# Performance work log

Hardware: AMD Instinct MI355X
Metric: run time of the kernel (lower is better)

The kernel has to match this reference:

```python
import jax, jax.numpy as jnp
import numpy as np
import math

FEATURE_DIMS = 6
D_HIDDEN = 32
N_TOKENS = 2097152
NUM_SEGMENTS = 8192
SCALE = 400.0 / math.log(10.0)


def setup_inputs() -> dict:
    key = jax.random.key(0)
    ks = jax.random.split(key, 8)
    x = jax.random.normal(ks[0], (N_TOKENS, FEATURE_DIMS), dtype=jnp.float32)
    segment_ids = jnp.sort(jax.random.randint(ks[1], (N_TOKENS,), 0, NUM_SEGMENTS)).astype(jnp.int32)
    # params (kaiming-ish init, same layout as nn.Linear: y = x @ W.T + b -> stored pre-transposed)
    W1 = jax.random.normal(ks[2], (FEATURE_DIMS, D_HIDDEN), dtype=jnp.float32) / np.sqrt(FEATURE_DIMS)
    b1 = jax.random.normal(ks[3], (D_HIDDEN,), dtype=jnp.float32) * 0.01
    wr = jax.random.normal(ks[4], (D_HIDDEN,), dtype=jnp.float32) / np.sqrt(D_HIDDEN)
    br = jax.random.normal(ks[5], (), dtype=jnp.float32) * 0.01
    wz = jax.random.normal(ks[6], (D_HIDDEN,), dtype=jnp.float32) / np.sqrt(D_HIDDEN)
    bz = jax.random.normal(ks[7], (), dtype=jnp.float32) * 0.01
    return {"x": x, "W1": W1, "b1": b1, "wr": wr, "br": br, "wz": wz, "bz": bz,
            "segment_ids": segment_ids, "num_segments": NUM_SEGMENTS}


def reference(x, W1, b1, wr, br, wz, bz, segment_ids, num_segments):
    # layer1: Linear + ReLU  -> h [N, d_hidden]
    h = jax.nn.relu(x @ W1 + b1)
    # rating / weight heads, squeezed to [N]
    r = h @ wr + br
    z = h @ wz + bz
    # per-segment (per-game) softmax over z, weighted sum of r -- single pass, no Python loop
    zmax = jax.ops.segment_max(z, segment_ids, num_segments=num_segments)  # [G], -inf for empty
    e = jnp.exp(z - zmax[segment_ids])                                      # [N]
    num = jax.ops.segment_sum(e * r, segment_ids, num_segments=num_segments)  # [G]
    den = jax.ops.segment_sum(e, segment_ids, num_segments=num_segments)      # [G]
    den_safe = jnp.where(den > 0, den, 1.0)
    preds = jnp.where(den > 0, num / den_safe, 0.0)  # empty segment -> 0, as in the torch code
    return SCALE * preds
```

## Files before the change

kernel.cpp:

```cpp
#include <hip/hip_runtime.h>

#define SCALE_F 173.71779276130078f
#define BLOCK 256
#define TPT 4

__global__ void zero_ws_kernel(float* __restrict__ ws, int n) {
    int i = blockIdx.x * 256 + threadIdx.x;
    if (i < n) ws[i] = 0.0f;
}

__global__ __launch_bounds__(BLOCK, 8) void strength_main_kernel(
    const float* __restrict__ x,
    const float* __restrict__ W1,
    const float* __restrict__ b1,
    const float* __restrict__ wr,
    const float* __restrict__ brp,
    const float* __restrict__ wz,
    const float* __restrict__ bzp,
    const int*   __restrict__ seg,
    int N,
    float* __restrict__ num,
    float* __restrict__ den)
{
    const int tid  = threadIdx.x;
    const int lane = tid & 63;

    const int t0   = blockIdx.x * (BLOCK * TPT) + tid * TPT;
    const int kmax = (t0 >= N) ? 0 : ((N - t0 < TPT) ? (N - t0) : TPT);

    float a[TPT * 6];
    int   sg[TPT];
    if (kmax == TPT) {
        const float4* xp = (const float4*)(x + (size_t)t0 * 6);
        #pragma unroll
        for (int i = 0; i < 6; ++i) {
            float4 v = xp[i];
            a[4 * i + 0] = v.x; a[4 * i + 1] = v.y;
            a[4 * i + 2] = v.z; a[4 * i + 3] = v.w;
        }
        int4 s0v = *(const int4*)(seg + t0);
        sg[0] = s0v.x; sg[1] = s0v.y; sg[2] = s0v.z; sg[3] = s0v.w;
    } else {
        #pragma unroll
        for (int k = 0; k < TPT; ++k) {
            if (k < kmax) {
                const float* xp = x + (size_t)(t0 + k) * 6;
                #pragma unroll
                for (int i = 0; i < 6; ++i) a[k * 6 + i] = xp[i];
                sg[k] = seg[t0 + k];
            } else {
                #pragma unroll
                for (int i = 0; i < 6; ++i) a[k * 6 + i] = 0.0f;
                sg[k] = -1;
            }
        }
    }

    const float brv = *brp;
    const float bzv = *bzp;

    float r[TPT], z[TPT];
    #pragma unroll
    for (int k = 0; k < TPT; ++k) { r[k] = brv; z[k] = bzv; }

    #pragma unroll 2
    for (int c = 0; c < 16; ++c) {
        const float2 w0 = *(const float2*)&W1[0 * 32 + 2 * c];
        const float2 w1 = *(const float2*)&W1[1 * 32 + 2 * c];
        const float2 w2 = *(const float2*)&W1[2 * 32 + 2 * c];
        const float2 w3 = *(const float2*)&W1[3 * 32 + 2 * c];
        const float2 w4 = *(const float2*)&W1[4 * 32 + 2 * c];
        const float2 w5 = *(const float2*)&W1[5 * 32 + 2 * c];
        const float2 bb = *(const float2*)&b1[2 * c];
        const float2 rr = *(const float2*)&wr[2 * c];
        const float2 zz = *(const float2*)&wz[2 * c];
        #pragma unroll
        for (int k = 0; k < TPT; ++k) {
            const float a0 = a[k*6+0], a1 = a[k*6+1], a2 = a[k*6+2];
            const float a3 = a[k*6+3], a4 = a[k*6+4], a5 = a[k*6+5];
            float h0 = fmaf(a0, w0.x, fmaf(a1, w1.x, fmaf(a2, w2.x,
                       fmaf(a3, w3.x, fmaf(a4, w4.x, fmaf(a5, w5.x, bb.x))))));
            float h1 = fmaf(a0, w0.y, fmaf(a1, w1.y, fmaf(a2, w2.y,
                       fmaf(a3, w3.y, fmaf(a4, w4.y, fmaf(a5, w5.y, bb.y))))));
            h0 = fmaxf(h0, 0.0f);
            h1 = fmaxf(h1, 0.0f);
            r[k] = fmaf(h0, rr.x, fmaf(h1, rr.y, r[k]));
            z[k] = fmaf(h0, zz.x, fmaf(h1, zz.y, z[k]));
        }
    }

    int   key = (kmax > 0) ? sg[0] : -1;
    float E = 0.0f, ER = 0.0f;
    #pragma unroll
    for (int k = 0; k < TPT; ++k) {
        if (k < kmax) {
            float e = __expf(z[k]);
            if (sg[k] != key) {
                atomicAdd(&den[key], E);
                atomicAdd(&num[key], ER);
                key = sg[k]; E = 0.0f; ER = 0.0f;
            }
            E += e; ER = fmaf(e, r[k], ER);
        }
    }

    #pragma unroll
    for (int d = 1; d < 64; d <<= 1) {
        int   k2 = __shfl_up(key, d);
        float E2 = __shfl_up(E,   d);
        float R2 = __shfl_up(ER,  d);
        if (lane >= d && k2 == key) { E += E2; ER += R2; }
    }
    int knext = __shfl_down(key, 1);
    bool last = (lane == 63) || (knext != key);
    if (last && key >= 0) {
        atomicAdd(&den[key], E);
        atomicAdd(&num[key], ER);
    }
}

__global__ void finalize_kernel(const float* __restrict__ num,
                                const float* __restrict__ den,
                                float* __restrict__ out, int G) {
    int g = blockIdx.x * 256 + threadIdx.x;
    if (g < G) {
        float d = den[g];
        out[g] = (d > 0.0f) ? (SCALE_F * num[g] / d) : 0.0f;
    }
}

extern "C" void kernel_launch(void* const* d_in, const int* in_sizes, int n_in,
                              void* d_out, int out_size, void* d_ws, size_t ws_size,
                              hipStream_t stream) {
    const float* x   = (const float*)d_in[0];
    const float* W1  = (const float*)d_in[1];
    const float* b1  = (const float*)d_in[2];
    const float* wr  = (const float*)d_in[3];
    const float* br  = (const float*)d_in[4];
    const float* wz  = (const float*)d_in[5];
    const float* bz  = (const float*)d_in[6];
    const int*   seg = (const int*)d_in[7];

    int N = in_sizes[7];
    int G = out_size;

    float* num = (float*)d_ws;
    float* den = num + G;
    float* out = (float*)d_out;

    int zn = 2 * G;
    zero_ws_kernel<<<(zn + 255) / 256, 256, 0, stream>>>(num, zn);

    long tokens_per_block = (long)BLOCK * TPT;
    int  nblocks = (int)(((long)N + tokens_per_block - 1) / tokens_per_block);
    strength_main_kernel<<<nblocks, BLOCK, 0, stream>>>(
        x, W1, b1, wr, br, wz, bz, seg, N, num, den);

    finalize_kernel<<<(G + 255) / 256, 256, 0, stream>>>(num, den, out, G);
}
```

Before: 30.47 us.

## Compute hidden layer with bf16 MFMA instead of scalar FMAs

Replaces the per-thread fp32 FMA evaluation of the 6x32 hidden layer with a 32x32x16 bf16 MFMA per wave. Each tile covers 32 tokens, with the bias folded in through a constant-one input column. The ReLU and the two head dot products are then reduced from the accumulator fragments with a cross-half shuffle. Token ownership changes to 8 consecutive tokens per lane across the lower half-wave, and occupancy bounds are loosened. This trades fp32 accuracy for bf16 inputs and uses strided, half-wave loads of x, which may hurt memory coalescing.

```diff
diff --git a/kernel.cpp b/kernel.cpp
--- a/kernel.cpp
+++ b/kernel.cpp
@@ -1,15 +1,27 @@
 #include <hip/hip_runtime.h>
+#include <hip/hip_bf16.h>
 
 #define SCALE_F 173.71779276130078f
 #define BLOCK 256
-#define TPT 4
+#define TILES 8
+
+typedef __attribute__((ext_vector_type(8)))  __bf16 bf16x8;
+typedef __attribute__((ext_vector_type(16))) float  f32x16;
+
+union FragU { unsigned u[4]; bf16x8 v; };
+
+__device__ inline unsigned pk_bf16(float lo, float hi) {
+    unsigned r;
+    asm("v_cvt_pk_bf16_f32 %0, %1, %2" : "=v"(r) : "v"(lo), "v"(hi));
+    return r;
+}
 
 __global__ void zero_ws_kernel(float* __restrict__ ws, int n) {
     int i = blockIdx.x * 256 + threadIdx.x;
     if (i < n) ws[i] = 0.0f;
 }
 
-__global__ __launch_bounds__(BLOCK, 8) void strength_main_kernel(
+__global__ __launch_bounds__(BLOCK, 4) void strength_mfma_kernel(
     const float* __restrict__ x,
     const float* __restrict__ W1,
     const float* __restrict__ b1,
@@ -22,85 +34,100 @@
     float* __restrict__ num,
     float* __restrict__ den)
 {
-    const int tid  = threadIdx.x;
-    const int lane = tid & 63;
+    const int  tid  = threadIdx.x;
+    const int  lane = tid & 63;
+    const int  l32  = lane & 31;
+    const bool lo   = (lane < 32);
 
-    const int t0   = blockIdx.x * (BLOCK * TPT) + tid * TPT;
-    const int kmax = (t0 >= N) ? 0 : ((N - t0 < TPT) ? (N - t0) : TPT);
+    const int wv    = blockIdx.x * (BLOCK / 64) + (tid >> 6);
+    const int wbase = wv * (32 * TILES);
+    if (wbase >= N) return;
+    const int tbase = wbase + l32 * TILES;
 
-    float a[TPT * 6];
-    int   sg[TPT];
-    if (kmax == TPT) {
-        const float4* xp = (const float4*)(x + (size_t)t0 * 6);
+    FragU A;
+    {
+        float w0=0.f,w1=0.f,w2=0.f,w3=0.f,w4=0.f,w5=0.f,bb=0.f;
+        if (lo) {
+            w0 = W1[0*32+l32]; w1 = W1[1*32+l32]; w2 = W1[2*32+l32];
+            w3 = W1[3*32+l32]; w4 = W1[4*32+l32]; w5 = W1[5*32+l32];
+            bb = b1[l32];
+        }
+        A.u[0] = pk_bf16(w0, w1);
+        A.u[1] = pk_bf16(w2, w3);
+        A.u[2] = pk_bf16(w4, w5);
+        A.u[3] = pk_bf16(bb, 0.f);
+    }
+
+    float wrv[16], wzv[16];
+    {
+        const int rb = (lane >> 5) * 4;
         #pragma unroll
-        for (int i = 0; i < 6; ++i) {
-            float4 v = xp[i];
-            a[4 * i + 0] = v.x; a[4 * i + 1] = v.y;
-            a[4 * i + 2] = v.z; a[4 * i + 3] = v.w;
+        for (int q = 0; q < 16; ++q) {
+            int row = (q & 3) + 8 * (q >> 2) + rb;
+            wrv[q] = wr[row];
+            wzv[q] = wz[row];
         }
-        int4 s0v = *(const int4*)(seg + t0);
-        sg[0] = s0v.x; sg[1] = s0v.y; sg[2] = s0v.z; sg[3] = s0v.w;
+    }
+
+    int sgid[8];
+    if (tbase + 8 <= N) {
+        int4 sa = *(const int4*)(seg + tbase);
+        int4 sb = *(const int4*)(seg + tbase + 4);
+        sgid[0]=sa.x; sgid[1]=sa.y; sgid[2]=sa.z; sgid[3]=sa.w;
+        sgid[4]=sb.x; sgid[5]=sb.y; sgid[6]=sb.z; sgid[7]=sb.w;
     } else {
         #pragma unroll
-        for (int k = 0; k < TPT; ++k) {
-            if (k < kmax) {
-                const float* xp = x + (size_t)(t0 + k) * 6;
-                #pragma unroll
-                for (int i = 0; i < 6; ++i) a[k * 6 + i] = xp[i];
-                sg[k] = seg[t0 + k];
-            } else {
-                #pragma unroll
-                for (int i = 0; i < 6; ++i) a[k * 6 + i] = 0.0f;
-                sg[k] = -1;
-            }
-        }
+        for (int t = 0; t < 8; ++t)
+            sgid[t] = (tbase + t < N) ? seg[tbase + t] : -1;
     }
 
     const float brv = *brp;
     const float bzv = *bzp;
 
-    float r[TPT], z[TPT];
-    #pragma unroll
-    for (int k = 0; k < TPT; ++k) { r[k] = brv; z[k] = bzv; }
+    int   key = -1;
+    float E = 0.f, ER = 0.f;
 
     #pragma unroll 2
-    for (int c = 0; c < 16; ++c) {
-        const float2 w0 = *(const float2*)&W1[0 * 32 + 2 * c];
-        const float2 w1 = *(const float2*)&W1[1 * 32 + 2 * c];
-        const float2 w2 = *(const float2*)&W1[2 * 32 + 2 * c];
-        const float2 w3 = *(const float2*)&W1[3 * 32 + 2 * c];
-        const float2 w4 = *(const float2*)&W1[4 * 32 + 2 * c];
-        const float2 w5 = *(const float2*)&W1[5 * 32 + 2 * c];
-        const float2 bb = *(const float2*)&b1[2 * c];
-        const float2 rr = *(const float2*)&wr[2 * c];
-        const float2 zz = *(const float2*)&wz[2 * c];
+    for (int t = 0; t < TILES; ++t) {
+        const int  token = tbase + t;
+        const bool ok    = lo && (token < N);
+
+        float2 p0 = {0.f,0.f}, p1 = {0.f,0.f}, p2 = {0.f,0.f};
+        if (ok) {
+            const float* xp = x + (size_t)token * 6;
+            p0 = *(const float2*)(xp + 0);
+            p1 = *(const float2*)(xp + 2);
+            p2 = *(const float2*)(xp + 4);
+        }
+        FragU B;
+        B.u[0] = pk_bf16(p0.x, p0.y);
+        B.u[1] = pk_bf16(p1.x, p1.y);
+        B.u[2] = pk_bf16(p2.x, p2.y);
+        B.u[3] = ok ? 0x00003F80u : 0u;
+
+        f32x16 acc = {0.f,0.f,0.f,0.f,0.f,0.f,0.f,0.f,
+                      0.f,0.f,0.f,0.f,0.f,0.f,0.f,0.f};
+        acc = __builtin_amdgcn_mfma_f32_32x32x16_bf16(A.v, B.v, acc, 0, 0, 0);
+
+        float rp = 0.f, zp = 0.f;
         #pragma unroll
-        for (int k = 0; k < TPT; ++k) {
-            const float a0 = a[k*6+0], a1 = a[k*6+1], a2 = a[k*6+2];
-            const float a3 = a[k*6+3], a4 = a[k*6+4], a5 = a[k*6+5];
-            float h0 = fmaf(a0, w0.x, fmaf(a1, w1.x, fmaf(a2, w2.x,
-                       fmaf(a3, w3.x, fmaf(a4, w4.x, fmaf(a5, w5.x, bb.x))))));
-            float h1 = fmaf(a0, w0.y, fmaf(a1, w1.y, fmaf(a2, w2.y,
-                       fmaf(a3, w3.y, fmaf(a4, w4.y, fmaf(a5, w5.y, bb.y))))));
-            h0 = fmaxf(h0, 0.0f);
-            h1 = fmaxf(h1, 0.0f);
-            r[k] = fmaf(h0, rr.x, fmaf(h1, rr.y, r[k]));
-            z[k] = fmaf(h0, zz.x, fmaf(h1, zz.y, z[k]));
+        for (int q = 0; q < 16; ++q) {
+            float h = fmaxf(acc[q], 0.f);
+            rp = fmaf(h, wrv[q], rp);
+            zp = fmaf(h, wzv[q], zp);
         }
-    }
+        rp += __shfl_xor(rp, 32);
+        zp += __shfl_xor(zp, 32);
 
-    int   key = (kmax > 0) ? sg[0] : -1;
-    float E = 0.0f, ER = 0.0f;
-    #pragma unroll
-    for (int k = 0; k < TPT; ++k) {
-        if (k < kmax) {
-            float e = __expf(z[k]);
-            if (sg[k] != key) {
-                atomicAdd(&den[key], E);
-                atomicAdd(&num[key], ER);
-                key = sg[k]; E = 0.0f; ER = 0.0f;
+        if (ok) {
+            float rt = rp + brv;
+            float e  = __expf(zp + bzv);
+            int   s  = sgid[t];
+            if (s != key) {
+                if (key >= 0) { atomicAdd(&den[key], E); atomicAdd(&num[key], ER); }
+                key = s; E = 0.f; ER = 0.f;
             }
-            E += e; ER = fmaf(e, r[k], ER);
+            E += e; ER = fmaf(e, rt, ER);
         }
     }
 
@@ -111,8 +138,8 @@
         float R2 = __shfl_up(ER,  d);
         if (lane >= d && k2 == key) { E += E2; ER += R2; }
     }
-    int knext = __shfl_down(key, 1);
-    bool last = (lane == 63) || (knext != key);
+    int  knext = __shfl_down(key, 1);
+    bool last  = (lane == 63) || (knext != key);
     if (last && key >= 0) {
         atomicAdd(&den[key], E);
         atomicAdd(&num[key], ER);
@@ -151,9 +178,9 @@
     int zn = 2 * G;
     zero_ws_kernel<<<(zn + 255) / 256, 256, 0, stream>>>(num, zn);
 
-    long tokens_per_block = (long)BLOCK * TPT;
+    long tokens_per_block = (long)(BLOCK / 64) * 32 * TILES;
     int  nblocks = (int)(((long)N + tokens_per_block - 1) / tokens_per_block);
-    strength_main_kernel<<<nblocks, BLOCK, 0, stream>>>(
+    strength_mfma_kernel<<<nblocks, BLOCK, 0, stream>>>(
         x, W1, b1, wr, br, wz, bz, seg, N, num, den);
 
     finalize_kernel<<<(G + 255) / 256, 256, 0, stream>>>(num, den, out, G);
```

After: 31.61 us. +3.7%, slower.
